# Performance work log

Hardware: AMD Instinct MI355X
Metric: run time of the kernel (lower is better)

## Reference

```python
import jax, jax.numpy as jnp
import numpy as np

B, T, E, H, M2 = 8, 2048, 256, 2, 134
HD = E // H


def setup_inputs() -> dict:
    key = jax.random.key(0)
    ks = jax.random.split(key, 10)
    s = 0.02
    return {
        "X": jax.random.normal(ks[0], (B, T, E), dtype=jnp.float32),
        "Y": jax.random.uniform(ks[1], (B, M2), dtype=jnp.float32),
        "wpe": s * jax.random.normal(ks[2], (T, E), dtype=jnp.float32),
        "ln1_g": jnp.ones((E,), jnp.float32), "ln1_b": jnp.zeros((E,), jnp.float32),
        "attn_w": s * jax.random.normal(ks[3], (3 * E, E), dtype=jnp.float32),
        "attn_b": jnp.zeros((3 * E,), jnp.float32),
        "attnproj_w": s * jax.random.normal(ks[4], (E, E), dtype=jnp.float32),
        "attnproj_b": jnp.zeros((E,), jnp.float32),
        "ln2_g": jnp.ones((E,), jnp.float32), "ln2_b": jnp.zeros((E,), jnp.float32),
        "fc_w": s * jax.random.normal(ks[5], (2 * E, E), dtype=jnp.float32),
        "fc_b": jnp.zeros((2 * E,), jnp.float32),
        "mlpproj_w": s * jax.random.normal(ks[6], (E, 2 * E), dtype=jnp.float32),
        "mlpproj_b": jnp.zeros((E,), jnp.float32),
        "lnf_g": jnp.ones((E,), jnp.float32), "lnf_b": jnp.zeros((E,), jnp.float32),
        "head_w": s * jax.random.normal(ks[7], (M2, E), dtype=jnp.float32),
        "head_b": jnp.zeros((M2,), jnp.float32),
    }


def _ln(x, g, b, eps=1e-5):
    mu = x.mean(-1, keepdims=True)
    var = ((x - mu) ** 2).mean(-1, keepdims=True)
    return (x - mu) * jax.lax.rsqrt(var + eps) * g + b


def reference(X, Y, wpe, ln1_g, ln1_b, attn_w, attn_b, attnproj_w, attnproj_b,
              ln2_g, ln2_b, fc_w, fc_b, mlpproj_w, mlpproj_b, lnf_g, lnf_b,
              head_w, head_b):
    # positional ids = arange(T) -> wpe itself; cls ids = [0]*T/2 + [1]*T/2
    cls_ids = np.concatenate([np.zeros(T // 2, np.int32), np.ones(T // 2, np.int32)])
    x = X + wpe + wpe[cls_ids]                      # [B,T,E] (dropout = identity, eval)

    # single Block (n_layer=1), preceded by ReLU as in cross_mod loop
    x = jax.nn.relu(x)
    h = _ln(x, ln1_g, ln1_b)
    qkv = h @ attn_w.T + attn_b                     # [B,T,3E]
    q, k, v = jnp.split(qkv, 3, axis=-1)
    q, k, v = jax.nn.relu(q), jax.nn.relu(k), jax.nn.relu(v)
    split_heads = lambda t: t.reshape(B, T, H, HD).transpose(0, 2, 1, 3)
    q, k, v = split_heads(q), split_heads(k), split_heads(v)
    att = jnp.einsum('bhqd,bhkd->bhqk', q, k) * (1.0 / np.sqrt(HD))
    tril = jnp.tril(jnp.ones((T, T), dtype=bool))
    # masked_fill(-inf) then ReLU  ==  zero outside causal mask, ReLU inside
    att = jnp.where(tril, jax.nn.relu(att), 0.0)    # [B,H,T,T]
    y = jnp.einsum('bhqk,bhkd->bhqd', att, v)
    y = y.transpose(0, 2, 1, 3).reshape(B, T, E)
    x = x + (y @ attnproj_w.T + attnproj_b)

    h = _ln(x, ln2_g, ln2_b)
    x = x + (jax.nn.relu(h @ fc_w.T + fc_b) @ mlpproj_w.T + mlpproj_b)

    x = jax.nn.relu(x)
    x = _ln(x, lnf_g, lnf_b)
    x = jax.nn.relu(x)
    emb = x.mean(axis=1)                            # [B,E]
    logits = jax.nn.relu(emb @ head_w.T + head_b)   # [B,M2]

    loss1 = jnp.sqrt(jnp.mean((logits - Y) ** 2))
    e1, e2 = emb[:, : E // 2], emb[:, E // 2:]
    loss3 = jnp.sqrt(jnp.mean((e1 - e2) ** 2))
    loss = 50.0 * loss1 + loss3
    return (e1, e2, loss, loss1, loss3, logits)
```

## Files before the change

kernel.cpp:

```cpp
#include <hip/hip_runtime.h>
#include <hip/hip_bf16.h>

#define Bc 8
#define Tc 2048
#define Ec 256
#define Hc 2
#define HDc 128
#define Mrows (Bc*Tc)
#define M2c 134

using bfx8  = __attribute__((ext_vector_type(8))) __bf16;
using f32x4 = __attribute__((ext_vector_type(4))) float;

__device__ __forceinline__ void gll16(const __bf16* g, __bf16* lds) {
    __builtin_amdgcn_global_load_lds(
        (const __attribute__((address_space(1))) unsigned int*)g,
        (__attribute__((address_space(3))) unsigned int*)lds, 16, 0, 0);
}

__global__ __launch_bounds__(256) void embed_prep_k(const float* X, const float* wpe,
                                                    const float* g, const float* bb,
                                                    const float* attn_w, const float* apw,
                                                    const float* fcw, const float* mpw,
                                                    __bf16* wb, float* embsum,
                                                    __bf16* xres, __bf16* hb) {
    int m = blockIdx.x;
    int e = threadIdx.x;
    if (m < 2048) {
        int i = m * 256 + e;
        if (i < 196608)       wb[i] = (__bf16)attn_w[i];
        else if (i < 262144)  wb[i] = (__bf16)apw[i - 196608];
        else if (i < 393216)  wb[i] = (__bf16)fcw[i - 262144];
        else                  wb[i] = (__bf16)mpw[i - 393216];
        if (m < 8) embsum[m * 256 + e] = 0.f;
    }
    int t = m & (Tc - 1);
    float v = X[(size_t)m * Ec + e] + wpe[(size_t)t * Ec + e] + wpe[(size_t)(t >= 1024) * Ec + e];
    v = fmaxf(v, 0.f);
    xres[(size_t)m * Ec + e] = (__bf16)v;
    float s1 = v, s2 = v * v;
    #pragma unroll
    for (int o = 32; o; o >>= 1) { s1 += __shfl_xor(s1, o, 64); s2 += __shfl_xor(s2, o, 64); }
    __shared__ float a1[4], a2[4];
    int w = threadIdx.x >> 6;
    if ((threadIdx.x & 63) == 0) { a1[w] = s1; a2[w] = s2; }
    __syncthreads();
    float m1 = (a1[0] + a1[1] + a1[2] + a1[3]) * (1.f / 256.f);
    float m2 = (a2[0] + a2[1] + a2[2] + a2[3]) * (1.f / 256.f);
    float r = rsqrtf(m2 - m1 * m1 + 1e-5f);
    hb[(size_t)m * Ec + e] = (__bf16)((v - m1) * r * g[e] + bb[e]);
}

__global__ __launch_bounds__(256) void gemm_qkv(const __bf16* __restrict__ A,
                                                const __bf16* __restrict__ Bw,
                                                const float* __restrict__ bias,
                                                __bf16* __restrict__ Qb,
                                                __bf16* __restrict__ Kb,
                                                unsigned short* __restrict__ Vt) {
    const int K = 256;
    __shared__ __bf16 As[128 * 64];
    __shared__ __bf16 Bs[128 * 64];
    __shared__ unsigned short trans[128][136];
    const int tid = threadIdx.x, w = tid >> 6, l = tid & 63;
    const int m0 = blockIdx.y * 128, n0 = blockIdx.x * 128;
    const int wr = w >> 1, wc = w & 1;
    const int quad = l >> 4, col15 = l & 15;
    const int isV = (n0 >= 512);

    f32x4 acc[4][4];
    f32x4 zz = {0.f, 0.f, 0.f, 0.f};
    #pragma unroll
    for (int i = 0; i < 4; i++)
        #pragma unroll
        for (int j = 0; j < 4; j++) acc[i][j] = zz;

    const int lrow = l >> 3;
    const int pbs  = l & 7;

    for (int kb = 0; kb < K; kb += 64) {
        #pragma unroll
        for (int it = 0; it < 4; it++) {
            int chunk = w * 4 + it;
            int row = chunk * 8 + lrow;
            int lb = pbs ^ (row & 7);
            gll16(A  + (size_t)(m0 + row) * K + kb + lb * 8, As + chunk * 512);
            gll16(Bw + (size_t)(n0 + row) * K + kb + lb * 8, Bs + chunk * 512);
        }
        __syncthreads();
        #pragma unroll
        for (int ks = 0; ks < 2; ks++) {
            bfx8 af[4], bfr[4];
            #pragma unroll
            for (int rt = 0; rt < 4; rt++) {
                int row = wr * 64 + rt * 16 + col15;
                int pb = (ks * 4 + quad) ^ (row & 7);
                af[rt] = *(const bfx8*)(As + row * 64 + pb * 8);
            }
            #pragma unroll
            for (int ct = 0; ct < 4; ct++) {
                int row = wc * 64 + ct * 16 + col15;
                int pb = (ks * 4 + quad) ^ (row & 7);
                bfr[ct] = *(const bfx8*)(Bs + row * 64 + pb * 8);
            }
            #pragma unroll
            for (int rt = 0; rt < 4; rt++)
                #pragma unroll
                for (int ct = 0; ct < 4; ct++)
                    acc[rt][ct] = __builtin_amdgcn_mfma_f32_16x16x32_bf16(af[rt], bfr[ct], acc[rt][ct], 0, 0, 0);
        }
        __syncthreads();
    }

    #pragma unroll
    for (int rt = 0; rt < 4; rt++)
        #pragma unroll
        for (int ct = 0; ct < 4; ct++) {
            int ng  = n0 + wc * 64 + ct * 16 + col15;
            float bsv = bias[ng];
            #pragma unroll
            for (int r = 0; r < 4; r++) {
                int mg = m0 + wr * 64 + rt * 16 + quad * 4 + r;
                float val = fmaxf(acc[rt][ct][r] + bsv, 0.f);
                __bf16 bv = (__bf16)val;
                if (isV) {
                    int d = ng & 127;
                    int tl = mg - m0;
                    trans[d][tl] = *(unsigned short*)&bv;
                } else {
                    int sel = ng >> 8;
                    int hh = (ng >> 7) & 1;
                    int d = ng & 127;
                    int bb = mg >> 11, tt = mg & (Tc - 1);
                    size_t idx = ((size_t)((bb * 2 + hh) * Tc + tt)) * HDc + d;
                    if (sel == 0) Qb[idx] = bv;
                    else Kb[idx] = bv;
                }
            }
        }
    if (isV) {
        __syncthreads();
        int h = (n0 >> 7) & 1;
        int b = m0 >> 11, t0 = m0 & (Tc - 1);
        int bh = b * 2 + h;
        int d = tid >> 1, th = tid & 1;
        unsigned short* dst = Vt + ((size_t)(bh * HDc + d)) * Tc + t0 + th * 64;
        const unsigned short* src = &trans[d][th * 64];
        #pragma unroll
        for (int i = 0; i < 8; i++)
            *(uint4*)(dst + i * 8) = *(const uint4*)(src + i * 8);
    }
}

__global__ __launch_bounds__(256, 4) void attn6_k(const __bf16* __restrict__ Qb,
                                                  const __bf16* __restrict__ Kb,
                                                  const __bf16* __restrict__ Vt,
                                                  __bf16* __restrict__ Y1,
                                                  __bf16* __restrict__ Y2,
                                                  __bf16* __restrict__ Y3,
                                                  __bf16* __restrict__ Y4) {
    __shared__ __bf16 Ks[64 * 128];
    __shared__ __bf16 Vs[128 * 64];
    __shared__ __bf16 Ss[64 * 64];
    int bid = blockIdx.x;
    int lane8 = bid & 7;
    int s = bid >> 3;
    int bh = ((s & 1) << 3) | lane8;
    int f = s >> 1;
    int qt, ch;
    if (f < 8)       { qt = f;                    ch = 0; }
    else if (f < 24) { qt = 8 + ((f - 8) >> 1);   ch = (f - 8) & 1; }
    else if (f < 48) { int r = f - 24; int d3 = r / 3; qt = 16 + d3; ch = r - 3 * d3; }
    else             { int r = f - 48; qt = 24 + (r >> 2); ch = r & 3; }
    int Q0 = qt * 64;
    int kts = ch * 8;
    int kte = min(kts + 8, qt + 1);

    int tid = threadIdx.x, w = tid >> 6, l = tid & 63;
    int quad = l >> 4, col15 = l & 15;
    const int lrowK = l >> 4, pbsK = l & 15;
    const int lrowV = l >> 3, pbsV = l & 7;

    #pragma unroll
    for (int it = 0; it < 4; it++) {
        int chunk = w * 4 + it;
        int row = chunk * 4 + lrowK;
        int lb = pbsK ^ (row & 7);
        gll16(Qb + ((size_t)(bh * Tc + Q0 + row)) * HDc + lb * 8, Ks + chunk * 512);
    }
    __syncthreads();
    bfx8 qf[4];
    #pragma unroll
    for (int ks = 0; ks < 4; ks++) {
        int row = w * 16 + col15;
        int pb = (ks * 4 + quad) ^ (row & 7);
        qf[ks] = *(const bfx8*)(Ks + row * 128 + pb * 8);
    }

    f32x4 zz = {0.f, 0.f, 0.f, 0.f};
    f32x4 yacc[8];
    #pragma unroll
    for (int i = 0; i < 8; i++) yacc[i] = zz;

    for (int kt = kts; kt < kte; kt++) {
        __syncthreads();
        #pragma unroll
        for (int it = 0; it < 4; it++) {
            int chunk = w * 4 + it;
            int rowK = chunk * 4 + lrowK;
            int lbK = pbsK ^ (rowK & 7);
            gll16(Kb + ((size_t)(bh * Tc + kt * 64 + rowK)) * HDc + lbK * 8, Ks + chunk * 512);
            int rowV = chunk * 8 + lrowV;
            int lbV = pbsV ^ (rowV & 7);
            gll16(Vt + ((size_t)(bh * HDc + rowV)) * Tc + kt * 64 + lbV * 8, Vs + chunk * 512);
        }
        __syncthreads();

        f32x4 sacc[4];
        #pragma unroll
        for (int i = 0; i < 4; i++) sacc[i] = zz;
        #pragma unroll
        for (int ks = 0; ks < 4; ks++) {
            #pragma unroll
            for (int ct = 0; ct < 4; ct++) {
                int row = ct * 16 + col15;
                int pb = (ks * 4 + quad) ^ (row & 7);
                bfx8 kf = *(const bfx8*)(Ks + row * 128 + pb * 8);
                sacc[ct] = __builtin_amdgcn_mfma_f32_16x16x32_bf16(qf[ks], kf, sacc[ct], 0, 0, 0);
            }
        }

        #pragma unroll
        for (int ct = 0; ct < 4; ct++) {
            int kl = ct * 16 + col15;
            int kg = kt * 64 + kl;
            int blk = kl >> 3, off = kl & 7;
            #pragma unroll
            for (int r = 0; r < 4; r++) {
                int qlw = w * 16 + quad * 4 + r;
                float val = (kg <= Q0 + qlw) ? fmaxf(sacc[ct][r], 0.f) : 0.f;
                int pb = blk ^ (qlw & 7);
                Ss[qlw * 64 + pb * 8 + off] = (__bf16)val;
            }
        }

        #pragma unroll
        for (int ks = 0; ks < 2; ks++) {
            int rowS = w * 16 + col15;
            int pbS = (ks * 4 + quad) ^ (rowS & 7);
            bfx8 sf = *(const bfx8*)(Ss + rowS * 64 + pbS * 8);
            #pragma unroll
            for (int dt = 0; dt < 8; dt++) {
                int row = dt * 16 + col15;
                int pb = (ks * 4 + quad) ^ (row & 7);
                bfx8 vf = *(const bfx8*)(Vs + row * 64 + pb * 8);
                yacc[dt] = __builtin_amdgcn_mfma_f32_16x16x32_bf16(sf, vf, yacc[dt], 0, 0, 0);
            }
        }
    }

    __bf16* Yp = (ch == 0) ? Y1 : (ch == 1) ? Y2 : (ch == 2) ? Y3 : Y4;
    int b = bh >> 1, h = bh & 1;
    const float sc = 0.08838834764831845f;
    #pragma unroll
    for (int dt = 0; dt < 8; dt++) {
        int d = dt * 16 + col15;
        #pragma unroll
        for (int r = 0; r < 4; r++) {
            int q = Q0 + w * 16 + quad * 4 + r;
            Yp[((size_t)(b * Tc + q)) * Ec + h * HDc + d] = (__bf16)(yacc[dt][r] * sc);
        }
    }
}

__global__ __launch_bounds__(256, 2) void mega_k(const __bf16* __restrict__ Y1,
                                                 const __bf16* __restrict__ Y2,
                                                 const __bf16* __restrict__ Y3,
                                                 const __bf16* __restrict__ Y4,
                                                 const __bf16* __restrict__ wap,
                                                 const float* __restrict__ apbias,
                                                 const __bf16* __restrict__ xres,
                                                 const float* __restrict__ ln2_g,
                                                 const float* __restrict__ ln2_b,
                                                 const __bf16* __restrict__ wfc,
                                                 const float* __restrict__ fcbias,
                                                 const __bf16* __restrict__ wmp,
                                                 const float* __restrict__ mpbias,
                                                 const float* __restrict__ lnf_g,
                                                 const float* __restrict__ lnf_b,
                                                 float* __restrict__ embsum) {
    __shared__ __bf16 fcs[32 * 512];
    __shared__ __bf16 h2s[32 * 256];
    __shared__ float red1[32][4], red2[32][4];
    __shared__ float cs[256];
    __bf16* As = fcs;

    const int tid = threadIdx.x, w = tid >> 6, l = tid & 63;
    const int m0 = blockIdx.x * 32;
    const int quad = l >> 4, col15 = l & 15;
    f32x4 zz = {0.f, 0.f, 0.f, 0.f};

    int qt = (m0 & (Tc - 1)) >> 6;
    int nsum = (qt + 8) >> 3;
    const __bf16* Ys[4] = {Y1, Y2, Y3, Y4};

    #pragma unroll
    for (int it = 0; it < 4; it++) {
        int idx = it * 256 + tid;
        int row = idx >> 5, blk = idx & 31;
        size_t off = (size_t)(m0 + row) * 256 + blk * 8;
        bfx8 a1 = *(const bfx8*)(Y1 + off);
        float tmp[8];
        #pragma unroll
        for (int jj = 0; jj < 8; jj++) tmp[jj] = (float)a1[jj];
        for (int j = 1; j < nsum; j++) {
            bfx8 aj = *(const bfx8*)(Ys[j] + off);
            #pragma unroll
            for (int jj = 0; jj < 8; jj++) tmp[jj] += (float)aj[jj];
        }
        #pragma unroll
        for (int jj = 0; jj < 8; jj++) a1[jj] = (__bf16)tmp[jj];
        *(bfx8*)(As + row * 256 + (blk ^ (row & 7)) * 8) = a1;
    }
    __syncthreads();

    f32x4 acc1[2][4];
    #pragma unroll
    for (int rt = 0; rt < 2; rt++)
        #pragma unroll
        for (int ct = 0; ct < 4; ct++) acc1[rt][ct] = zz;
    #pragma unroll
    for (int kw = 0; kw < 8; kw++) {
        bfx8 af[2], bf[4];
        #pragma unroll
        for (int rt = 0; rt < 2; rt++) {
            int row = rt * 16 + col15;
            int pb = (kw * 4 + quad) ^ (row & 7);
            af[rt] = *(const bfx8*)(As + row * 256 + pb * 8);
        }
        #pragma unroll
        for (int ct = 0; ct < 4; ct++)
            bf[ct] = *(const bfx8*)(wap + (size_t)(w * 64 + ct * 16 + col15) * 256 + kw * 32 + quad * 8);
        #pragma unroll
        for (int rt = 0; rt < 2; rt++)
            #pragma unroll
            for (int ct = 0; ct < 4; ct++)
                acc1[rt][ct] = __builtin_amdgcn_mfma_f32_16x16x32_bf16(af[rt], bf[ct], acc1[rt][ct], 0, 0, 0);
    }

    float xv[2][4][4];
    #pragma unroll
    for (int rt = 0; rt < 2; rt++)
        #pragma unroll
        for (int ct = 0; ct < 4; ct++) {
            int ng = w * 64 + ct * 16 + col15;
            float bsv = apbias[ng];
            #pragma unroll
            for (int r = 0; r < 4; r++) {
                int mg = m0 + rt * 16 + quad * 4 + r;
                xv[rt][ct][r] = acc1[rt][ct][r] + bsv + (float)xres[(size_t)mg * 256 + ng];
            }
        }
    #pragma unroll
    for (int rt = 0; rt < 2; rt++)
        #pragma unroll
        for (int r = 0; r < 4; r++) {
            float a = 0.f, b2 = 0.f;
            #pragma unroll
            for (int ct = 0; ct < 4; ct++) { a += xv[rt][ct][r]; b2 += xv[rt][ct][r] * xv[rt][ct][r]; }
            #pragma unroll
            for (int o = 1; o < 16; o <<= 1) { a += __shfl_xor(a, o, 64); b2 += __shfl_xor(b2, o, 64); }
            if (col15 == 0) {
                int row = rt * 16 + quad * 4 + r;
                red1[row][w] = a; red2[row][w] = b2;
            }
        }
    __syncthreads();
    #pragma unroll
    for (int rt = 0; rt < 2; rt++)
        #pragma unroll
        for (int r = 0; r < 4; r++) {
            int row = rt * 16 + quad * 4 + r;
            float s1 = red1[row][0] + red1[row][1] + red1[row][2] + red1[row][3];
            float s2 = red2[row][0] + red2[row][1] + red2[row][2] + red2[row][3];
            float mu = s1 * (1.f / 256.f);
            float var = s2 * (1.f / 256.f) - mu * mu;
            float rs = rsqrtf(var + 1e-5f);
            #pragma unroll
            for (int ct = 0; ct < 4; ct++) {
                int ng = w * 64 + ct * 16 + col15;
                float h = (xv[rt][ct][r] - mu) * rs * ln2_g[ng] + ln2_b[ng];
                h2s[row * 256 + ((ng >> 3) ^ (row & 7)) * 8 + (ng & 7)] = (__bf16)h;
            }
        }
    __syncthreads();

    for (int g2 = 0; g2 < 2; g2++) {
        f32x4 acc2[2][4];
        #pragma unroll
        for (int rt = 0; rt < 2; rt++)
            #pragma unroll
            for (int ct = 0; ct < 4; ct++) acc2[rt][ct] = zz;
        #pragma unroll
        for (int kw = 0; kw < 8; kw++) {
            bfx8 af[2], bf[4];
            #pragma unroll
            for (int rt = 0; rt < 2; rt++) {
                int row = rt * 16 + col15;
                int pb = (kw * 4 + quad) ^ (row & 7);
                af[rt] = *(const bfx8*)(h2s + row * 256 + pb * 8);
            }
            #pragma unroll
            for (int ct = 0; ct < 4; ct++)
                bf[ct] = *(const bfx8*)(wfc + (size_t)(w * 128 + g2 * 64 + ct * 16 + col15) * 256 + kw * 32 + quad * 8);
            #pragma unroll
            for (int rt = 0; rt < 2; rt++)
                #pragma unroll
                for (int ct = 0; ct < 4; ct++)
                    acc2[rt][ct] = __builtin_amdgcn_mfma_f32_16x16x32_bf16(af[rt], bf[ct], acc2[rt][ct], 0, 0, 0);
        }
        #pragma unroll
        for (int rt = 0; rt < 2; rt++)
            #pragma unroll
            for (int ct = 0; ct < 4; ct++) {
                int col = w * 128 + g2 * 64 + ct * 16 + col15;
                float bsv = fcbias[col];
                #pragma unroll
                for (int r = 0; r < 4; r++) {
                    int row = rt * 16 + quad * 4 + r;
                    float val = fmaxf(acc2[rt][ct][r] + bsv, 0.f);
                    fcs[row * 512 + ((col >> 3) ^ (row & 7)) * 8 + (col & 7)] = (__bf16)val;
                }
            }
    }
    __syncthreads();

    f32x4 acc3[2][4];
    #pragma unroll
    for (int rt = 0; rt < 2; rt++)
        #pragma unroll
        for (int ct = 0; ct < 4; ct++) acc3[rt][ct] = zz;
    #pragma unroll
    for (int kw = 0; kw < 16; kw++) {
        bfx8 af[2], bf[4];
        #pragma unroll
        for (int rt = 0; rt < 2; rt++) {
            int row = rt * 16 + col15;
            int pb = (kw * 4 + quad) ^ (row & 7);
            af[rt] = *(const bfx8*)(fcs + row * 512 + pb * 8);
        }
        #pragma unroll
        for (int ct = 0; ct < 4; ct++)
            bf[ct] = *(const bfx8*)(wmp + (size_t)(w * 64 + ct * 16 + col15) * 512 + kw * 32 + quad * 8);
        #pragma unroll
        for (int rt = 0; rt < 2; rt++)
            #pragma unroll
            for (int ct = 0; ct < 4; ct++)
                acc3[rt][ct] = __builtin_amdgcn_mfma_f32_16x16x32_bf16(af[rt], bf[ct], acc3[rt][ct], 0, 0, 0);
    }

    #pragma unroll
    for (int rt = 0; rt < 2; rt++)
        #pragma unroll
        for (int ct = 0; ct < 4; ct++) {
            int ng = w * 64 + ct * 16 + col15;
            float bsv = mpbias[ng];
            #pragma unroll
            for (int r = 0; r < 4; r++)
                xv[rt][ct][r] = fmaxf(acc3[rt][ct][r] + bsv + xv[rt][ct][r], 0.f);
        }
    __syncthreads();
    #pragma unroll
    for (int rt = 0; rt < 2; rt++)
        #pragma unroll
        for (int r = 0; r < 4; r++) {
            float a = 0.f, b2 = 0.f;
            #pragma unroll
            for (int ct = 0; ct < 4; ct++) { a += xv[rt][ct][r]; b2 += xv[rt][ct][r] * xv[rt][ct][r]; }
            #pragma unroll
            for (int o = 1; o < 16; o <<= 1) { a += __shfl_xor(a, o, 64); b2 += __shfl_xor(b2, o, 64); }
            if (col15 == 0) {
                int row = rt * 16 + quad * 4 + r;
                red1[row][w] = a; red2[row][w] = b2;
            }
        }
    __syncthreads();
    float colsum[4] = {0.f, 0.f, 0.f, 0.f};
    #pragma unroll
    for (int rt = 0; rt < 2; rt++)
        #pragma unroll
        for (int r = 0; r < 4; r++) {
            int row = rt * 16 + quad * 4 + r;
            float s1 = red1[row][0] + red1[row][1] + red1[row][2] + red1[row][3];
            float s2 = red2[row][0] + red2[row][1] + red2[row][2] + red2[row][3];
            float mu = s1 * (1.f / 256.f);
            float var = s2 * (1.f / 256.f) - mu * mu;
            float rs = rsqrtf(var + 1e-5f);
            #pragma unroll
            for (int ct = 0; ct < 4; ct++) {
                int ng = w * 64 + ct * 16 + col15;
                float h = (xv[rt][ct][r] - mu) * rs * lnf_g[ng] + lnf_b[ng];
                colsum[ct] += fmaxf(h, 0.f);
            }
        }
    #pragma unroll
    for (int ct = 0; ct < 4; ct++) {
        colsum[ct] += __shfl_xor(colsum[ct], 16, 64);
        colsum[ct] += __shfl_xor(colsum[ct], 32, 64);
    }
    if (quad == 0) {
        #pragma unroll
        for (int ct = 0; ct < 4; ct++)
            cs[w * 64 + ct * 16 + col15] = colsum[ct];
    }
    __syncthreads();
    atomicAdd(&embsum[(m0 >> 11) * 256 + tid], cs[tid]);
}

__global__ __launch_bounds__(256) void final_k(const float* embsum, const float* Yt,
                                               const float* head_w, const float* head_b,
                                               float* out) {
    __shared__ float semb[2048];
    __shared__ float slog[1072];
    int tid = threadIdx.x;
    for (int i = tid; i < 2048; i += 256) semb[i] = embsum[i] * (1.f / 2048.f);
    __syncthreads();
    float part1 = 0.f;
    for (int idx = tid; idx < 1072; idx += 256) {
        int b = idx / M2c, n = idx - b * M2c;
        float acc = head_b[n];
        const float* wn = head_w + (size_t)n * Ec;
        const float* e = semb + b * Ec;
        #pragma unroll 8
        for (int k = 0; k < Ec; k++) acc += e[k] * wn[k];
        acc = fmaxf(acc, 0.f);
        slog[idx] = acc;
        float d = acc - Yt[idx];
        part1 += d * d;
    }
    float part3 = 0.f;
    for (int idx = tid; idx < 1024; idx += 256) {
        int b = idx >> 7, i = idx & 127;
        float d = semb[b * Ec + i] - semb[b * Ec + 128 + i];
        part3 += d * d;
    }
    #pragma unroll
    for (int o = 32; o; o >>= 1) { part1 += __shfl_xor(part1, o, 64); part3 += __shfl_xor(part3, o, 64); }
    __shared__ float r1[4], r3[4];
    int w = tid >> 6;
    if ((tid & 63) == 0) { r1[w] = part1; r3[w] = part3; }
    __syncthreads();
    float l1 = sqrtf((r1[0] + r1[1] + r1[2] + r1[3]) / 1072.f);
    float l3 = sqrtf((r3[0] + r3[1] + r3[2] + r3[3]) / 1024.f);
    for (int idx = tid; idx < 1024; idx += 256) {
        int b = idx >> 7, i = idx & 127;
        out[idx]        = semb[b * Ec + i];
        out[1024 + idx] = semb[b * Ec + 128 + i];
    }
    if (tid == 0) {
        out[2048] = 50.f * l1 + l3;
        out[2049] = l1;
        out[2050] = l3;
    }
    for (int idx = tid; idx < 1072; idx += 256) out[2051 + idx] = slog[idx];
}

extern "C" void kernel_launch(void* const* d_in, const int* in_sizes, int n_in,
                              void* d_out, int out_size, void* d_ws, size_t ws_size,
                              hipStream_t stream) {
    const float* X        = (const float*)d_in[0];
    const float* Yt       = (const float*)d_in[1];
    const float* wpe      = (const float*)d_in[2];
    const float* ln1_g    = (const float*)d_in[3];
    const float* ln1_b    = (const float*)d_in[4];
    const float* attn_w   = (const float*)d_in[5];
    const float* attn_b   = (const float*)d_in[6];
    const float* apw      = (const float*)d_in[7];
    const float* apb      = (const float*)d_in[8];
    const float* ln2_g    = (const float*)d_in[9];
    const float* ln2_b    = (const float*)d_in[10];
    const float* fcw      = (const float*)d_in[11];
    const float* fcb      = (const float*)d_in[12];
    const float* mpw      = (const float*)d_in[13];
    const float* mpb      = (const float*)d_in[14];
    const float* lnf_g    = (const float*)d_in[15];
    const float* lnf_b    = (const float*)d_in[16];
    const float* head_w   = (const float*)d_in[17];
    const float* head_b   = (const float*)d_in[18];

    char* ws = (char*)d_ws;
    const size_t MB = 1048576;
    __bf16* xres   = (__bf16*)(ws + 0 * MB);
    __bf16* hb     = (__bf16*)(ws + 8 * MB);
    __bf16* Qb     = (__bf16*)(ws + 16 * MB);
    __bf16* Kb     = (__bf16*)(ws + 24 * MB);
    __bf16* Vb     = (__bf16*)(ws + 32 * MB);
    __bf16* Vt     = (__bf16*)(ws + 40 * MB);
    __bf16* Y1     = (__bf16*)(ws + 48 * MB);
    __bf16* Y2     = (__bf16*)(ws + 56 * MB);
    __bf16* wb     = (__bf16*)(ws + 64 * MB);
    float*  embsum = (float*)(ws + 65 * MB);

    __bf16* Y3 = hb;
    __bf16* Y4 = Vb;

    __bf16* wqkv = wb;
    __bf16* wap  = wb + 196608;
    __bf16* wfc  = wb + 262144;
    __bf16* wmp  = wb + 393216;

    embed_prep_k<<<Mrows, 256, 0, stream>>>(X, wpe, ln1_g, ln1_b,
                                            attn_w, apw, fcw, mpw, wb, embsum, xres, hb);
    gemm_qkv<<<dim3(6, 128), 256, 0, stream>>>(hb, wqkv, attn_b, Qb, Kb, (unsigned short*)Vt);
    attn6_k<<<1280, 256, 0, stream>>>(Qb, Kb, Vt, Y1, Y2, Y3, Y4);
    mega_k<<<512, 256, 0, stream>>>(Y1, Y2, Y3, Y4, wap, apb, xres, ln2_g, ln2_b,
                                    wfc, fcb, wmp, mpb, lnf_g, lnf_b, embsum);
    final_k<<<1, 256, 0, stream>>>(embsum, Yt, head_w, head_b, (float*)d_out);
}
```

Baseline: 252.9 us.

## Fuse final head into mega kernel via last-block counter and prefetch weights

```diff
diff --git a/kernel.cpp b/kernel.cpp
--- a/kernel.cpp
+++ b/kernel.cpp
@@ -33,6 +33,7 @@
         else if (i < 393216)  wb[i] = (__bf16)fcw[i - 262144];
         else                  wb[i] = (__bf16)mpw[i - 393216];
         if (m < 8) embsum[m * 256 + e] = 0.f;
+        if (m == 8 && e == 0) ((unsigned int*)embsum)[2048] = 0u;
     }
     int t = m & (Tc - 1);
     float v = X[(size_t)m * Ec + e] + wpe[(size_t)t * Ec + e] + wpe[(size_t)(t >= 1024) * Ec + e];
@@ -287,11 +288,16 @@
                                                  const float* __restrict__ mpbias,
                                                  const float* __restrict__ lnf_g,
                                                  const float* __restrict__ lnf_b,
-                                                 float* __restrict__ embsum) {
+                                                 float* __restrict__ embsum,
+                                                 const float* __restrict__ Yt,
+                                                 const float* __restrict__ head_w,
+                                                 const float* __restrict__ head_b,
+                                                 float* __restrict__ out) {
     __shared__ __bf16 fcs[32 * 512];
     __shared__ __bf16 h2s[32 * 256];
     __shared__ float red1[32][4], red2[32][4];
     __shared__ float cs[256];
+    __shared__ int lastFlag;
     __bf16* As = fcs;
 
     const int tid = threadIdx.x, w = tid >> 6, l = tid & 63;
@@ -328,23 +334,36 @@
     for (int rt = 0; rt < 2; rt++)
         #pragma unroll
         for (int ct = 0; ct < 4; ct++) acc1[rt][ct] = zz;
-    #pragma unroll
-    for (int kw = 0; kw < 8; kw++) {
-        bfx8 af[2], bf[4];
-        #pragma unroll
-        for (int rt = 0; rt < 2; rt++) {
-            int row = rt * 16 + col15;
-            int pb = (kw * 4 + quad) ^ (row & 7);
-            af[rt] = *(const bfx8*)(As + row * 256 + pb * 8);
-        }
-        #pragma unroll
-        for (int ct = 0; ct < 4; ct++)
-            bf[ct] = *(const bfx8*)(wap + (size_t)(w * 64 + ct * 16 + col15) * 256 + kw * 32 + quad * 8);
-        #pragma unroll
-        for (int rt = 0; rt < 2; rt++)
-            #pragma unroll
-            for (int ct = 0; ct < 4; ct++)
-                acc1[rt][ct] = __builtin_amdgcn_mfma_f32_16x16x32_bf16(af[rt], bf[ct], acc1[rt][ct], 0, 0, 0);
+    {
+        const __bf16* bp0 = wap + (size_t)(w * 64 + 0 * 16 + col15) * 256 + quad * 8;
+        const __bf16* bp1 = wap + (size_t)(w * 64 + 1 * 16 + col15) * 256 + quad * 8;
+        const __bf16* bp2 = wap + (size_t)(w * 64 + 2 * 16 + col15) * 256 + quad * 8;
+        const __bf16* bp3 = wap + (size_t)(w * 64 + 3 * 16 + col15) * 256 + quad * 8;
+        const __bf16* bptr[4] = {bp0, bp1, bp2, bp3};
+        bfx8 bp[2][4];
+        #pragma unroll
+        for (int ct = 0; ct < 4; ct++) bp[0][ct] = *(const bfx8*)(bptr[ct]);
+        #pragma unroll
+        for (int kw = 0; kw < 8; kw++) {
+            int cur = kw & 1;
+            if (kw + 1 < 8) {
+                #pragma unroll
+                for (int ct = 0; ct < 4; ct++)
+                    bp[cur ^ 1][ct] = *(const bfx8*)(bptr[ct] + (kw + 1) * 32);
+            }
+            bfx8 af[2];
+            #pragma unroll
+            for (int rt = 0; rt < 2; rt++) {
+                int row = rt * 16 + col15;
+                int pb = (kw * 4 + quad) ^ (row & 7);
+                af[rt] = *(const bfx8*)(As + row * 256 + pb * 8);
+            }
+            #pragma unroll
+            for (int rt = 0; rt < 2; rt++)
+                #pragma unroll
+                for (int ct = 0; ct < 4; ct++)
+                    acc1[rt][ct] = __builtin_amdgcn_mfma_f32_16x16x32_bf16(af[rt], bp[cur][ct], acc1[rt][ct], 0, 0, 0);
+        }
     }
 
     float xv[2][4][4];
@@ -400,9 +419,22 @@
         for (int rt = 0; rt < 2; rt++)
             #pragma unroll
             for (int ct = 0; ct < 4; ct++) acc2[rt][ct] = zz;
+        const __bf16* bptr[4];
+        #pragma unroll
+        for (int ct = 0; ct < 4; ct++)
+            bptr[ct] = wfc + (size_t)(w * 128 + g2 * 64 + ct * 16 + col15) * 256 + quad * 8;
+        bfx8 bp[2][4];
+        #pragma unroll
+        for (int ct = 0; ct < 4; ct++) bp[0][ct] = *(const bfx8*)(bptr[ct]);
         #pragma unroll
         for (int kw = 0; kw < 8; kw++) {
-            bfx8 af[2], bf[4];
+            int cur = kw & 1;
+            if (kw + 1 < 8) {
+                #pragma unroll
+                for (int ct = 0; ct < 4; ct++)
+                    bp[cur ^ 1][ct] = *(const bfx8*)(bptr[ct] + (kw + 1) * 32);
+            }
+            bfx8 af[2];
             #pragma unroll
             for (int rt = 0; rt < 2; rt++) {
                 int row = rt * 16 + col15;
@@ -410,13 +442,10 @@
                 af[rt] = *(const bfx8*)(h2s + row * 256 + pb * 8);
             }
             #pragma unroll
-            for (int ct = 0; ct < 4; ct++)
-                bf[ct] = *(const bfx8*)(wfc + (size_t)(w * 128 + g2 * 64 + ct * 16 + col15) * 256 + kw * 32 + quad * 8);
-            #pragma unroll
             for (int rt = 0; rt < 2; rt++)
                 #pragma unroll
                 for (int ct = 0; ct < 4; ct++)
-                    acc2[rt][ct] = __builtin_amdgcn_mfma_f32_16x16x32_bf16(af[rt], bf[ct], acc2[rt][ct], 0, 0, 0);
+                    acc2[rt][ct] = __builtin_amdgcn_mfma_f32_16x16x32_bf16(af[rt], bp[cur][ct], acc2[rt][ct], 0, 0, 0);
         }
         #pragma unroll
         for (int rt = 0; rt < 2; rt++)
@@ -439,23 +468,35 @@
     for (int rt = 0; rt < 2; rt++)
         #pragma unroll
         for (int ct = 0; ct < 4; ct++) acc3[rt][ct] = zz;
-    #pragma unroll
-    for (int kw = 0; kw < 16; kw++) {
-        bfx8 af[2], bf[4];
-        #pragma unroll
-        for (int rt = 0; rt < 2; rt++) {
-            int row = rt * 16 + col15;
-            int pb = (kw * 4 + quad) ^ (row & 7);
-            af[rt] = *(const bfx8*)(fcs + row * 512 + pb * 8);
-        }
+    {
+        const __bf16* bptr[4];
         #pragma unroll
         for (int ct = 0; ct < 4; ct++)
-            bf[ct] = *(const bfx8*)(wmp + (size_t)(w * 64 + ct * 16 + col15) * 512 + kw * 32 + quad * 8);
-        #pragma unroll
-        for (int rt = 0; rt < 2; rt++)
-            #pragma unroll
-            for (int ct = 0; ct < 4; ct++)
-                acc3[rt][ct] = __builtin_amdgcn_mfma_f32_16x16x32_bf16(af[rt], bf[ct], acc3[rt][ct], 0, 0, 0);
+            bptr[ct] = wmp + (size_t)(w * 64 + ct * 16 + col15) * 512 + quad * 8;
+        bfx8 bp[2][4];
+        #pragma unroll
+        for (int ct = 0; ct < 4; ct++) bp[0][ct] = *(const bfx8*)(bptr[ct]);
+        #pragma unroll
+        for (int kw = 0; kw < 16; kw++) {
+            int cur = kw & 1;
+            if (kw + 1 < 16) {
+                #pragma unroll
+                for (int ct = 0; ct < 4; ct++)
+                    bp[cur ^ 1][ct] = *(const bfx8*)(bptr[ct] + (kw + 1) * 32);
+            }
+            bfx8 af[2];
+            #pragma unroll
+            for (int rt = 0; rt < 2; rt++) {
+                int row = rt * 16 + col15;
+                int pb = (kw * 4 + quad) ^ (row & 7);
+                af[rt] = *(const bfx8*)(fcs + row * 512 + pb * 8);
+            }
+            #pragma unroll
+            for (int rt = 0; rt < 2; rt++)
+                #pragma unroll
+                for (int ct = 0; ct < 4; ct++)
+                    acc3[rt][ct] = __builtin_amdgcn_mfma_f32_16x16x32_bf16(af[rt], bp[cur][ct], acc3[rt][ct], 0, 0, 0);
+        }
     }
 
     #pragma unroll
@@ -514,54 +555,61 @@
     }
     __syncthreads();
     atomicAdd(&embsum[(m0 >> 11) * 256 + tid], cs[tid]);
-}
-
-__global__ __launch_bounds__(256) void final_k(const float* embsum, const float* Yt,
-                                               const float* head_w, const float* head_b,
-                                               float* out) {
-    __shared__ float semb[2048];
-    __shared__ float slog[1072];
-    int tid = threadIdx.x;
-    for (int i = tid; i < 2048; i += 256) semb[i] = embsum[i] * (1.f / 2048.f);
-    __syncthreads();
-    float part1 = 0.f;
-    for (int idx = tid; idx < 1072; idx += 256) {
-        int b = idx / M2c, n = idx - b * M2c;
-        float acc = head_b[n];
-        const float* wn = head_w + (size_t)n * Ec;
-        const float* e = semb + b * Ec;
-        #pragma unroll 8
-        for (int k = 0; k < Ec; k++) acc += e[k] * wn[k];
-        acc = fmaxf(acc, 0.f);
-        slog[idx] = acc;
-        float d = acc - Yt[idx];
-        part1 += d * d;
-    }
-    float part3 = 0.f;
-    for (int idx = tid; idx < 1024; idx += 256) {
-        int b = idx >> 7, i = idx & 127;
-        float d = semb[b * Ec + i] - semb[b * Ec + 128 + i];
-        part3 += d * d;
-    }
-    #pragma unroll
-    for (int o = 32; o; o >>= 1) { part1 += __shfl_xor(part1, o, 64); part3 += __shfl_xor(part3, o, 64); }
-    __shared__ float r1[4], r3[4];
-    int w = tid >> 6;
-    if ((tid & 63) == 0) { r1[w] = part1; r3[w] = part3; }
-    __syncthreads();
-    float l1 = sqrtf((r1[0] + r1[1] + r1[2] + r1[3]) / 1072.f);
-    float l3 = sqrtf((r3[0] + r3[1] + r3[2] + r3[3]) / 1024.f);
-    for (int idx = tid; idx < 1024; idx += 256) {
-        int b = idx >> 7, i = idx & 127;
-        out[idx]        = semb[b * Ec + i];
-        out[1024 + idx] = semb[b * Ec + 128 + i];
-    }
+
+    __syncthreads();
     if (tid == 0) {
-        out[2048] = 50.f * l1 + l3;
-        out[2049] = l1;
-        out[2050] = l3;
-    }
-    for (int idx = tid; idx < 1072; idx += 256) out[2051 + idx] = slog[idx];
+        __threadfence();
+        unsigned old = atomicAdd((unsigned int*)(embsum + 2048), 1u);
+        lastFlag = (old == 511u);
+    }
+    __syncthreads();
+    if (!lastFlag) return;
+
+    {
+        float* semb = (float*)fcs;
+        float* slog = semb + 2048;
+        for (int i = tid; i < 2048; i += 256)
+            semb[i] = atomicAdd(&embsum[i], 0.f) * (1.f / 2048.f);
+        __syncthreads();
+        float part1 = 0.f;
+        for (int idx = tid; idx < 1072; idx += 256) {
+            int b = idx / M2c, n = idx - b * M2c;
+            float acc = head_b[n];
+            const float* wn = head_w + (size_t)n * Ec;
+            const float* e = semb + b * Ec;
+            #pragma unroll 8
+            for (int k = 0; k < Ec; k++) acc += e[k] * wn[k];
+            acc = fmaxf(acc, 0.f);
+            slog[idx] = acc;
+            float d = acc - Yt[idx];
+            part1 += d * d;
+        }
+        float part3 = 0.f;
+        for (int idx = tid; idx < 1024; idx += 256) {
+            int b = idx >> 7, i = idx & 127;
+            float d = semb[b * Ec + i] - semb[b * Ec + 128 + i];
+            part3 += d * d;
+        }
+        #pragma unroll
+        for (int o = 32; o; o >>= 1) { part1 += __shfl_xor(part1, o, 64); part3 += __shfl_xor(part3, o, 64); }
+        __syncthreads();
+        int ww = tid >> 6;
+        if ((tid & 63) == 0) { red1[0][ww] = part1; red1[1][ww] = part3; }
+        __syncthreads();
+        float l1 = sqrtf((red1[0][0] + red1[0][1] + red1[0][2] + red1[0][3]) / 1072.f);
+        float l3 = sqrtf((red1[1][0] + red1[1][1] + red1[1][2] + red1[1][3]) / 1024.f);
+        for (int idx = tid; idx < 1024; idx += 256) {
+            int b = idx >> 7, i = idx & 127;
+            out[idx]        = semb[b * Ec + i];
+            out[1024 + idx] = semb[b * Ec + 128 + i];
+        }
+        if (tid == 0) {
+            out[2048] = 50.f * l1 + l3;
+            out[2049] = l1;
+            out[2050] = l3;
+        }
+        for (int idx = tid; idx < 1072; idx += 256) out[2051 + idx] = slog[idx];
+    }
 }
 
 extern "C" void kernel_launch(void* const* d_in, const int* in_sizes, int n_in,
@@ -613,6 +661,6 @@
     gemm_qkv<<<dim3(6, 128), 256, 0, stream>>>(hb, wqkv, attn_b, Qb, Kb, (unsigned short*)Vt);
     attn6_k<<<1280, 256, 0, stream>>>(Qb, Kb, Vt, Y1, Y2, Y3, Y4);
     mega_k<<<512, 256, 0, stream>>>(Y1, Y2, Y3, Y4, wap, apb, xres, ln2_g, ln2_b,
-                                    wfc, fcb, wmp, mpb, lnf_g, lnf_b, embsum);
-    final_k<<<1, 256, 0, stream>>>(embsum, Yt, head_w, head_b, (float*)d_out);
+                                    wfc, fcb, wmp, mpb, lnf_g, lnf_b, embsum,
+                                    Yt, head_w, head_b, (float*)d_out);
 }
```

Measured after the change: 257.5 us. No clear change (+1.8%).
